# Kernel tuning notes

Hardware: AMD Instinct MI355X
Metric: run time of the kernel (lower is better)

The kernel has to match this reference:

```python
import jax, jax.numpy as jnp
import numpy as np

D_MODEL = 256

def setup_inputs() -> dict:
    key = jax.random.key(0)
    k_x, k_wqkv, k_bqkv, k_wp, k_bp = jax.random.split(key, 5)
    B, T, d = 4, 4096, D_MODEL
    bound_qkv = 1.0 / np.sqrt(d)
    return {
        "x": jax.random.normal(k_x, (B, T, d), dtype=jnp.float32),
        "W_qkv": jax.random.uniform(k_wqkv, (d, 3 * d), jnp.float32, -bound_qkv, bound_qkv),
        "b_qkv": jax.random.uniform(k_bqkv, (3 * d,), jnp.float32, -bound_qkv, bound_qkv),
        "W_proj": jax.random.uniform(k_wp, (d, d), jnp.float32, -bound_qkv, bound_qkv),
        "b_proj": jax.random.uniform(k_bp, (d,), jnp.float32, -bound_qkv, bound_qkv),
    }

def reference(x, W_qkv, b_qkv, W_proj, b_proj):
    B, T, d = x.shape
    qkv = x @ W_qkv + b_qkv                       # (B, T, 3d)
    q, k, v = jnp.split(qkv, 3, axis=-1)          # each (B, T, d)
    scale = 1.0 / np.sqrt(d).astype(np.float32)
    scores = jnp.einsum('btd,bsd->bts', q, k) * scale   # (B, T, T)
    causal = jnp.tril(jnp.ones((T, T), dtype=bool))     # allowed positions
    scores = jnp.where(causal, scores, -jnp.inf)
    weights = jax.nn.softmax(scores, axis=-1)           # (B, T, T)
    ctx = jnp.einsum('bts,bsd->btd', weights, v)        # (B, T, d)
    return ctx @ W_proj + b_proj
```

## Files before the change

kernel.cpp:

```cpp
#include <hip/hip_runtime.h>
#include <math.h>

#define TT 4096
#define BB 4
#define DM 256
#define NSEG_B 288

typedef __attribute__((ext_vector_type(8))) short short8;
typedef __attribute__((ext_vector_type(4))) short short4v;
typedef __attribute__((ext_vector_type(4))) float f32x4;

#define MFMA16(a, b, c) __builtin_amdgcn_mfma_f32_16x16x32_bf16(a, b, c, 0, 0, 0)

#define GL2LDS(gp, lp) __builtin_amdgcn_global_load_lds( \
    (const __attribute__((address_space(1))) unsigned int*)(gp), \
    (__attribute__((address_space(3))) unsigned int*)(lp), 16, 0, 0)

__device__ __forceinline__ short f2b(float f) {
    union { float f; unsigned u; } v; v.f = f;
    unsigned r = v.u + 0x7FFFu + ((v.u >> 16) & 1u);
    return (short)(r >> 16);
}

__global__ __launch_bounds__(256) void transpose_cast2(
    const float* __restrict__ W1, short* __restrict__ Wt1,
    const float* __restrict__ W2, short* __restrict__ Wt2)
{
    __shared__ float T[64 * 68];
    const int tid = threadIdx.x;
    const int by = blockIdx.y;
    const float* W; short* Wt; int N, n0;
    if (by < 12) { W = W1; Wt = Wt1; N = 768; n0 = by * 64; }
    else         { W = W2; Wt = Wt2; N = 256; n0 = (by - 12) * 64; }
    const int k0 = blockIdx.x * 64;
#pragma unroll
    for (int it = 0; it < 4; ++it) {
        int idx = tid + it * 256;
        int r = idx >> 4, c4 = idx & 15;
        *(float4*)&T[r * 68 + c4 * 4] =
            *(const float4*)&W[(size_t)(k0 + r) * N + n0 + c4 * 4];
    }
    __syncthreads();
#pragma unroll
    for (int it = 0; it < 4; ++it) {
        int idx = tid + it * 256;
        int n = idx >> 4, c4 = idx & 15;
        short4v t;
#pragma unroll
        for (int j = 0; j < 4; ++j) t[j] = f2b(T[(c4 * 4 + j) * 68 + n]);
        *(short4v*)&Wt[(size_t)(n0 + n) * 256 + k0 + c4 * 4] = t;
    }
}

__global__ __launch_bounds__(256) void qkv_gemm(
    const float* __restrict__ x, const short* __restrict__ Bt,
    const float* __restrict__ bias, short* __restrict__ qkvb,
    short* __restrict__ VtG)
{
    __shared__ short As[16384];
    __shared__ short Bs[16384];
    __shared__ short Ts[64 * 72];

    const int tid = threadIdx.x;
    const int w = tid >> 6, lane = tid & 63;
    const int l15 = lane & 15, quad = lane >> 4;
    const int m0 = blockIdx.x * 64;
    const int nsup = blockIdx.y * 384;

#pragma unroll
    for (int it = 0; it < 8; ++it) {
        int idx = tid + it * 256;
        int row = ((idx >> 9) << 4) + (idx & 15);
        int col = ((idx >> 6) & 7) * 32 + ((idx >> 4) & 3) * 8;
        const float* src = &x[(size_t)(m0 + row) * 256 + col];
        float4 u = *(const float4*)src, u2 = *(const float4*)(src + 4);
        short8 t;
        t[0] = f2b(u.x);  t[1] = f2b(u.y);  t[2] = f2b(u.z);  t[3] = f2b(u.w);
        t[4] = f2b(u2.x); t[5] = f2b(u2.y); t[6] = f2b(u2.z); t[7] = f2b(u2.w);
        *(short8*)&As[idx * 8] = t;
    }

    for (int t6 = 0; t6 < 6; ++t6) {
        const int n0 = nsup + t6 * 64;
#pragma unroll
        for (int it = 0; it < 8; ++it) {
            int idx = tid + it * 256;
            int n = ((idx >> 9) << 4) + (idx & 15);
            int col = ((idx >> 6) & 7) * 32 + ((idx >> 4) & 3) * 8;
            *(short8*)&Bs[idx * 8] = *(const short8*)&Bt[(size_t)(n0 + n) * 256 + col];
        }
        __syncthreads();

        f32x4 acc[4];
#pragma unroll
        for (int t = 0; t < 4; ++t) acc[t] = (f32x4){0.f, 0.f, 0.f, 0.f};
#pragma unroll
        for (int k0 = 0; k0 < 8; ++k0) {
            short8 a = *(const short8*)&As[((w * 8 + k0) * 64 + lane) * 8];
#pragma unroll
            for (int nt = 0; nt < 4; ++nt) {
                short8 bb = *(const short8*)&Bs[((nt * 8 + k0) * 64 + lane) * 8];
                acc[nt] = MFMA16(a, bb, acc[nt]);
            }
        }

        if (n0 < 512) {
#pragma unroll
            for (int nt = 0; nt < 4; ++nt) {
                int n = n0 + nt * 16 + l15;
                float bv = bias[n];
#pragma unroll
                for (int r = 0; r < 4; ++r)
                    qkvb[(size_t)(m0 + w * 16 + quad * 4 + r) * 768 + n]
                        = f2b(acc[nt][r] + bv);
            }
            __syncthreads();
        } else {
#pragma unroll
            for (int nt = 0; nt < 4; ++nt) {
                int n = n0 + nt * 16 + l15;
                float bv = bias[n];
#pragma unroll
                for (int r = 0; r < 4; ++r)
                    Ts[(nt * 16 + l15) * 72 + w * 16 + quad * 4 + r]
                        = f2b(acc[nt][r] + bv);
            }
            __syncthreads();
            const int d  = tid >> 2;
            const int c  = tid & 3;
            short8 v0 = *(const short8*)&Ts[d * 72 + c * 16];
            short8 v1 = *(const short8*)&Ts[d * 72 + c * 16 + 8];
            const int bg = m0 >> 12, key0 = (m0 & 4095) + c * 16;
            short* dst = &VtG[((size_t)bg * 256 + (n0 - 512) + d) * 4096 + key0];
            *(short8*)dst = v0;
            *(short8*)(dst + 8) = v1;
        }
    }
}

__global__ __launch_bounds__(256, 3) void flash_mfma(
    const short* __restrict__ qkv,
    const short* __restrict__ VtG,
    float* __restrict__ Opart,
    float* __restrict__ L)
{
    __shared__ short Ks[2][4096];
    __shared__ short Vs[2][8192];
    __shared__ short Ps[2048];

    const int tid = threadIdx.x;
    const int w = tid >> 6, lane = tid & 63;
    const int l15 = lane & 15, quad = lane >> 4;

    const int b = blockIdx.x & 3;
    const int e = (NSEG_B - 1) - (blockIdx.x >> 2);
    const int lid = b * NSEG_B + e;
    int g = 0;
    while (g < 7 && e >= 4 * (g + 1) * (g + 2)) ++g;
    int off = e - 4 * g * (g + 1);
    int qt = 8 * g + off / (g + 1);
    int s  = off - (off / (g + 1)) * (g + 1);
    const int kp_lo = s * 16;
    const int kp_hi = min(kp_lo + 16, 2 * (qt + 1));
    const int npairs = kp_hi - kp_lo;

    const size_t base = (size_t)b * TT * 768;
    const int row0 = qt * 64;

    short8 aq[8];
    {
        const short* qrow = &qkv[base + (size_t)(row0 + w * 16 + l15) * 768 + quad * 8];
#pragma unroll
        for (int k0 = 0; k0 < 8; ++k0)
            aq[k0] = *(const short8*)&qrow[k0 * 32];
    }

#pragma unroll
    for (int it = 0; it < 2; ++it) {
        int idx = tid + it * 256;
        int row = idx & 15;
        int col = ((idx >> 6) & 7) * 32 + ((idx >> 4) & 3) * 8;
        GL2LDS(&qkv[base + (size_t)(kp_lo * 32 + row) * 768 + 256 + col], &Ks[0][idx * 8]);
    }
#pragma unroll
    for (int it = 0; it < 4; ++it) {
        int idx = tid + it * 256;
        int d  = ((idx >> 6) << 4) + (idx & 15);
        int kc = ((idx >> 4) & 3) * 8;
        GL2LDS(&VtG[((size_t)b * 256 + d) * 4096 + kp_lo * 32 + kc], &Vs[0][idx * 8]);
    }

    f32x4 o[16];
#pragma unroll
    for (int c = 0; c < 16; ++c) o[c] = (f32x4){0.f, 0.f, 0.f, 0.f};
    float l_acc[4] = {0.f, 0.f, 0.f, 0.f};

    for (int u = 0; u < npairs; ++u) {
        const int j0 = (kp_lo + u) * 32;

        __syncthreads();

#pragma unroll
        for (int it = 0; it < 2; ++it) {
            int idx = tid + it * 256;
            int row = idx & 15;
            int col = ((idx >> 6) & 7) * 32 + ((idx >> 4) & 3) * 8;
            GL2LDS(&qkv[base + (size_t)(j0 + 16 + row) * 768 + 256 + col], &Ks[1][idx * 8]);
        }
        if (u + 1 < npairs) {
#pragma unroll
            for (int it = 0; it < 4; ++it) {
                int idx = tid + it * 256;
                int d  = ((idx >> 6) << 4) + (idx & 15);
                int kc = ((idx >> 4) & 3) * 8;
                GL2LDS(&VtG[((size_t)b * 256 + d) * 4096 + j0 + 32 + kc],
                       &Vs[(u + 1) & 1][idx * 8]);
            }
        }

        {
            f32x4 s4 = (f32x4){0.f, 0.f, 0.f, 0.f};
#pragma unroll
            for (int k0 = 0; k0 < 8; ++k0) {
                short8 bb = *(const short8*)&Ks[0][(k0 * 64 + lane) * 8];
                s4 = MFMA16(aq[k0], bb, s4);
            }
#pragma unroll
            for (int r = 0; r < 4; ++r) {
                const int rg = row0 + w * 16 + quad * 4 + r;
                int jg = j0 + l15;
                float xx = s4[r] * 0.0625f;
                if (jg > rg) xx = -INFINITY;
                float pv = __expf(fminf(xx, 30.f));
                l_acc[r] += pv;
                Ps[(w * 64 + (l15 >> 3) * 16 + quad * 4 + r) * 8 + (l15 & 7)] = f2b(pv);
            }
        }

        __syncthreads();

        if (u + 1 < npairs) {
#pragma unroll
            for (int it = 0; it < 2; ++it) {
                int idx = tid + it * 256;
                int row = idx & 15;
                int col = ((idx >> 6) & 7) * 32 + ((idx >> 4) & 3) * 8;
                GL2LDS(&qkv[base + (size_t)(j0 + 32 + row) * 768 + 256 + col], &Ks[0][idx * 8]);
            }
        }

        {
            f32x4 s4 = (f32x4){0.f, 0.f, 0.f, 0.f};
#pragma unroll
            for (int k0 = 0; k0 < 8; ++k0) {
                short8 bb = *(const short8*)&Ks[1][(k0 * 64 + lane) * 8];
                s4 = MFMA16(aq[k0], bb, s4);
            }
#pragma unroll
            for (int r = 0; r < 4; ++r) {
                const int rg = row0 + w * 16 + quad * 4 + r;
                int jg = j0 + 16 + l15;
                float xx = s4[r] * 0.0625f;
                if (jg > rg) xx = -INFINITY;
                float pv = __expf(fminf(xx, 30.f));
                l_acc[r] += pv;
                Ps[(w * 64 + (2 + (l15 >> 3)) * 16 + quad * 4 + r) * 8 + (l15 & 7)] = f2b(pv);
            }
        }

        {
            short8 a0 = *(const short8*)&Ps[(w * 64 + lane) * 8];
#pragma unroll
            for (int ct = 0; ct < 16; ++ct) {
                short8 bb = *(const short8*)&Vs[u & 1][(ct * 64 + lane) * 8];
                o[ct] = MFMA16(a0, bb, o[ct]);
            }
        }
    }

#pragma unroll
    for (int r = 0; r < 4; ++r) {
        float l = l_acc[r];
        l += __shfl_xor(l, 1); l += __shfl_xor(l, 2);
        l += __shfl_xor(l, 4); l += __shfl_xor(l, 8);
        if (l15 == 0)
            L[(size_t)lid * 64 + w * 16 + quad * 4 + r] = l;
    }
    const size_t ob = (size_t)lid * (64 * 256);
#pragma unroll
    for (int r = 0; r < 4; ++r) {
        int lr = w * 16 + quad * 4 + r;
#pragma unroll
        for (int c = 0; c < 16; ++c)
            Opart[ob + (size_t)lr * 256 + c * 16 + l15] = o[c][r];
    }
}

__global__ __launch_bounds__(256) void proj_gemm(
    const float* __restrict__ Opart, const float* __restrict__ L,
    const short* __restrict__ Bt, const float* __restrict__ bias,
    float* __restrict__ out)
{
    __shared__ short As[16384];
    __shared__ short Bs[16384];
    __shared__ float Linv[64];

    const int tid = threadIdx.x;
    const int w = tid >> 6, lane = tid & 63;
    const int l15 = lane & 15, quad = lane >> 4;
    const int t = blockIdx.x;
    const int b = t >> 6, qt = t & 63;
    const int gg = qt >> 3, rr = qt & 7;
    const int sbase = b * NSEG_B + 4 * gg * (gg + 1) + rr * (gg + 1);
    const int nseg = gg + 1;
    const int m0 = t * 64;

    if (tid < 64) {
        float l = 0.f;
#pragma unroll
        for (int s2 = 0; s2 < 8; ++s2)
            if (s2 < nseg) l += L[(size_t)(sbase + s2) * 64 + tid];
        Linv[tid] = 1.f / l;
    }
    __syncthreads();

#pragma unroll
    for (int it = 0; it < 8; ++it) {
        int idx = tid + it * 256;
        int row = ((idx >> 9) << 4) + (idx & 15);
        int col = ((idx >> 6) & 7) * 32 + ((idx >> 4) & 3) * 8;
        float a8[8] = {0.f, 0.f, 0.f, 0.f, 0.f, 0.f, 0.f, 0.f};
#pragma unroll
        for (int s2 = 0; s2 < 8; ++s2) {
            if (s2 < nseg) {
                const float* src = &Opart[(size_t)(sbase + s2) * 16384
                                          + (size_t)row * 256 + col];
                float4 u = *(const float4*)src, u2 = *(const float4*)(src + 4);
                a8[0] += u.x;  a8[1] += u.y;  a8[2] += u.z;  a8[3] += u.w;
                a8[4] += u2.x; a8[5] += u2.y; a8[6] += u2.z; a8[7] += u2.w;
            }
        }
        float inv = Linv[row];
        short8 t8;
#pragma unroll
        for (int j = 0; j < 8; ++j) t8[j] = f2b(a8[j] * inv);
        *(short8*)&As[idx * 8] = t8;
    }

    for (int t2 = 0; t2 < 2; ++t2) {
        const int n0 = blockIdx.y * 128 + t2 * 64;
#pragma unroll
        for (int it = 0; it < 8; ++it) {
            int idx = tid + it * 256;
            int n = ((idx >> 9) << 4) + (idx & 15);
            int col = ((idx >> 6) & 7) * 32 + ((idx >> 4) & 3) * 8;
            *(short8*)&Bs[idx * 8] = *(const short8*)&Bt[(size_t)(n0 + n) * 256 + col];
        }
        __syncthreads();

        f32x4 acc[4];
#pragma unroll
        for (int tt = 0; tt < 4; ++tt) acc[tt] = (f32x4){0.f, 0.f, 0.f, 0.f};
#pragma unroll
        for (int k0 = 0; k0 < 8; ++k0) {
            short8 a = *(const short8*)&As[((w * 8 + k0) * 64 + lane) * 8];
#pragma unroll
            for (int nt = 0; nt < 4; ++nt) {
                short8 bb = *(const short8*)&Bs[((nt * 8 + k0) * 64 + lane) * 8];
                acc[nt] = MFMA16(a, bb, acc[nt]);
            }
        }
#pragma unroll
        for (int nt = 0; nt < 4; ++nt) {
            int n = n0 + nt * 16 + l15;
            float bv = bias[n];
#pragma unroll
            for (int r = 0; r < 4; ++r)
                out[(size_t)(m0 + w * 16 + quad * 4 + r) * 256 + n] = acc[nt][r] + bv;
        }
        __syncthreads();
    }
}

extern "C" void kernel_launch(void* const* d_in, const int* in_sizes, int n_in,
                              void* d_out, int out_size, void* d_ws, size_t ws_size,
                              hipStream_t stream)
{
    const float* x     = (const float*)d_in[0];
    const float* Wqkv  = (const float*)d_in[1];
    const float* bqkv  = (const float*)d_in[2];
    const float* Wproj = (const float*)d_in[3];
    const float* bproj = (const float*)d_in[4];
    float* out = (float*)d_out;

    const size_t M = (size_t)BB * TT;
    short* qkv_b = (short*)d_ws;
    short* Wt1   = qkv_b + M * 768;
    short* Wt2   = Wt1 + (size_t)768 * 256;
    short* VtG   = Wt2 + (size_t)256 * 256;
    float* Opart = (float*)(VtG + (size_t)BB * 256 * 4096);
    float* L     = Opart + (size_t)BB * NSEG_B * 64 * 256;

    dim3 blk(256);
    transpose_cast2<<<dim3(4, 16), blk, 0, stream>>>(Wqkv, Wt1, Wproj, Wt2);
    qkv_gemm<<<dim3(256, 2), blk, 0, stream>>>(x, Wt1, bqkv, qkv_b, VtG);
    flash_mfma<<<dim3(BB * NSEG_B), blk, 0, stream>>>(qkv_b, VtG, Opart, L);
    proj_gemm<<<dim3(256, 2), blk, 0, stream>>>(Opart, L, Wt2, bproj, out);
}
```

Measured before the change: 226.6 us.

## Widen flash attention tiles to 128 query rows with 512-thread blocks

The flash kernel now processes 128 query rows per block using 8 waves, which halves the number of key/value tile loads per query row and halves the segment count. One block barrier per key pair is replaced by an explicit vmcnt wait plus s_barrier, with sched_barriers to pin the order of async LDS loads relative to compute. The projection GEMM is re-tiled to 32-row blocks covering all 256 output columns to match the new partial layout. The risks are lower occupancy from the larger blocks, fewer blocks to balance across CUs, and fragile hand-written waitcnt counts.

```diff
diff --git a/kernel.cpp b/kernel.cpp
--- a/kernel.cpp
+++ b/kernel.cpp
@@ -4,7 +4,7 @@
 #define TT 4096
 #define BB 4
 #define DM 256
-#define NSEG_B 288
+#define NSEG_B 144
 
 typedef __attribute__((ext_vector_type(8))) short short8;
 typedef __attribute__((ext_vector_type(4))) short short4v;
@@ -138,7 +138,7 @@
     }
 }
 
-__global__ __launch_bounds__(256, 3) void flash_mfma(
+__global__ __launch_bounds__(512, 2) void flash_mfma(
     const short* __restrict__ qkv,
     const short* __restrict__ VtG,
     float* __restrict__ Opart,
@@ -146,7 +146,7 @@
 {
     __shared__ short Ks[2][4096];
     __shared__ short Vs[2][8192];
-    __shared__ short Ps[2048];
+    __shared__ short Ps[4096];
 
     const int tid = threadIdx.x;
     const int w = tid >> 6, lane = tid & 63;
@@ -156,16 +156,16 @@
     const int e = (NSEG_B - 1) - (blockIdx.x >> 2);
     const int lid = b * NSEG_B + e;
     int g = 0;
-    while (g < 7 && e >= 4 * (g + 1) * (g + 2)) ++g;
-    int off = e - 4 * g * (g + 1);
-    int qt = 8 * g + off / (g + 1);
+    while (g < 7 && e >= 2 * (g + 1) * (g + 2)) ++g;
+    int off = e - 2 * g * (g + 1);
+    int qt = 4 * g + off / (g + 1);
     int s  = off - (off / (g + 1)) * (g + 1);
     const int kp_lo = s * 16;
-    const int kp_hi = min(kp_lo + 16, 2 * (qt + 1));
+    const int kp_hi = min(kp_lo + 16, 4 * (qt + 1));
     const int npairs = kp_hi - kp_lo;
 
     const size_t base = (size_t)b * TT * 768;
-    const int row0 = qt * 64;
+    const int row0 = qt * 128;
 
     short8 aq[8];
     {
@@ -175,16 +175,16 @@
             aq[k0] = *(const short8*)&qrow[k0 * 32];
     }
 
-#pragma unroll
-    for (int it = 0; it < 2; ++it) {
-        int idx = tid + it * 256;
+    {
+        int idx = tid;
         int row = idx & 15;
         int col = ((idx >> 6) & 7) * 32 + ((idx >> 4) & 3) * 8;
         GL2LDS(&qkv[base + (size_t)(kp_lo * 32 + row) * 768 + 256 + col], &Ks[0][idx * 8]);
     }
-#pragma unroll
-    for (int it = 0; it < 4; ++it) {
-        int idx = tid + it * 256;
+    __builtin_amdgcn_sched_barrier(0);
+#pragma unroll
+    for (int it = 0; it < 2; ++it) {
+        int idx = tid + it * 512;
         int d  = ((idx >> 6) << 4) + (idx & 15);
         int kc = ((idx >> 4) & 3) * 8;
         GL2LDS(&VtG[((size_t)b * 256 + d) * 4096 + kp_lo * 32 + kc], &Vs[0][idx * 8]);
@@ -200,23 +200,24 @@
 
         __syncthreads();
 
-#pragma unroll
-        for (int it = 0; it < 2; ++it) {
-            int idx = tid + it * 256;
+        {
+            int idx = tid;
             int row = idx & 15;
             int col = ((idx >> 6) & 7) * 32 + ((idx >> 4) & 3) * 8;
             GL2LDS(&qkv[base + (size_t)(j0 + 16 + row) * 768 + 256 + col], &Ks[1][idx * 8]);
         }
+        __builtin_amdgcn_sched_barrier(0);
         if (u + 1 < npairs) {
 #pragma unroll
-            for (int it = 0; it < 4; ++it) {
-                int idx = tid + it * 256;
+            for (int it = 0; it < 2; ++it) {
+                int idx = tid + it * 512;
                 int d  = ((idx >> 6) << 4) + (idx & 15);
                 int kc = ((idx >> 4) & 3) * 8;
                 GL2LDS(&VtG[((size_t)b * 256 + d) * 4096 + j0 + 32 + kc],
                        &Vs[(u + 1) & 1][idx * 8]);
             }
         }
+        __builtin_amdgcn_sched_barrier(0);
 
         {
             f32x4 s4 = (f32x4){0.f, 0.f, 0.f, 0.f};
@@ -237,17 +238,21 @@
             }
         }
 
-        __syncthreads();
-
         if (u + 1 < npairs) {
-#pragma unroll
-            for (int it = 0; it < 2; ++it) {
-                int idx = tid + it * 256;
-                int row = idx & 15;
-                int col = ((idx >> 6) & 7) * 32 + ((idx >> 4) & 3) * 8;
-                GL2LDS(&qkv[base + (size_t)(j0 + 32 + row) * 768 + 256 + col], &Ks[0][idx * 8]);
-            }
-        }
+            asm volatile("s_waitcnt vmcnt(2)" ::: "memory");
+        } else {
+            asm volatile("s_waitcnt vmcnt(0)" ::: "memory");
+        }
+        __builtin_amdgcn_s_barrier();
+        __builtin_amdgcn_sched_barrier(0);
+
+        if (u + 1 < npairs) {
+            int idx = tid;
+            int row = idx & 15;
+            int col = ((idx >> 6) & 7) * 32 + ((idx >> 4) & 3) * 8;
+            GL2LDS(&qkv[base + (size_t)(j0 + 32 + row) * 768 + 256 + col], &Ks[0][idx * 8]);
+        }
+        __builtin_amdgcn_sched_barrier(0);
 
         {
             f32x4 s4 = (f32x4){0.f, 0.f, 0.f, 0.f};
@@ -284,9 +289,9 @@
         l += __shfl_xor(l, 1); l += __shfl_xor(l, 2);
         l += __shfl_xor(l, 4); l += __shfl_xor(l, 8);
         if (l15 == 0)
-            L[(size_t)lid * 64 + w * 16 + quad * 4 + r] = l;
-    }
-    const size_t ob = (size_t)lid * (64 * 256);
+            L[(size_t)lid * 128 + w * 16 + quad * 4 + r] = l;
+    }
+    const size_t ob = (size_t)lid * (128 * 256);
 #pragma unroll
     for (int r = 0; r < 4; ++r) {
         int lr = w * 16 + quad * 4 + r;
@@ -301,31 +306,33 @@
     const short* __restrict__ Bt, const float* __restrict__ bias,
     float* __restrict__ out)
 {
-    __shared__ short As[16384];
+    __shared__ short As[8192];
     __shared__ short Bs[16384];
-    __shared__ float Linv[64];
+    __shared__ float Linv[32];
 
     const int tid = threadIdx.x;
     const int w = tid >> 6, lane = tid & 63;
     const int l15 = lane & 15, quad = lane >> 4;
     const int t = blockIdx.x;
-    const int b = t >> 6, qt = t & 63;
-    const int gg = qt >> 3, rr = qt & 7;
-    const int sbase = b * NSEG_B + 4 * gg * (gg + 1) + rr * (gg + 1);
+    const int b = t >> 7, q32 = t & 127;
+    const int qt = q32 >> 2;
+    const int ro = (q32 & 3) * 32;
+    const int gg = qt >> 2, rr = qt & 3;
+    const int sbase = b * NSEG_B + 2 * gg * (gg + 1) + rr * (gg + 1);
     const int nseg = gg + 1;
-    const int m0 = t * 64;
-
-    if (tid < 64) {
+    const int m0 = t * 32;
+
+    if (tid < 32) {
         float l = 0.f;
 #pragma unroll
         for (int s2 = 0; s2 < 8; ++s2)
-            if (s2 < nseg) l += L[(size_t)(sbase + s2) * 64 + tid];
+            if (s2 < nseg) l += L[(size_t)(sbase + s2) * 128 + ro + tid];
         Linv[tid] = 1.f / l;
     }
     __syncthreads();
 
 #pragma unroll
-    for (int it = 0; it < 8; ++it) {
+    for (int it = 0; it < 4; ++it) {
         int idx = tid + it * 256;
         int row = ((idx >> 9) << 4) + (idx & 15);
         int col = ((idx >> 6) & 7) * 32 + ((idx >> 4) & 3) * 8;
@@ -333,8 +340,8 @@
 #pragma unroll
         for (int s2 = 0; s2 < 8; ++s2) {
             if (s2 < nseg) {
-                const float* src = &Opart[(size_t)(sbase + s2) * 16384
-                                          + (size_t)row * 256 + col];
+                const float* src = &Opart[(size_t)(sbase + s2) * 32768
+                                          + (size_t)(ro + row) * 256 + col];
                 float4 u = *(const float4*)src, u2 = *(const float4*)(src + 4);
                 a8[0] += u.x;  a8[1] += u.y;  a8[2] += u.z;  a8[3] += u.w;
                 a8[4] += u2.x; a8[5] += u2.y; a8[6] += u2.z; a8[7] += u2.w;
@@ -347,8 +354,8 @@
         *(short8*)&As[idx * 8] = t8;
     }
 
-    for (int t2 = 0; t2 < 2; ++t2) {
-        const int n0 = blockIdx.y * 128 + t2 * 64;
+    for (int t2 = 0; t2 < 4; ++t2) {
+        const int n0 = t2 * 64;
 #pragma unroll
         for (int it = 0; it < 8; ++it) {
             int idx = tid + it * 256;
@@ -358,25 +365,26 @@
         }
         __syncthreads();
 
-        f32x4 acc[4];
-#pragma unroll
-        for (int tt = 0; tt < 4; ++tt) acc[tt] = (f32x4){0.f, 0.f, 0.f, 0.f};
+        f32x4 acc[2];
+        acc[0] = (f32x4){0.f, 0.f, 0.f, 0.f};
+        acc[1] = (f32x4){0.f, 0.f, 0.f, 0.f};
 #pragma unroll
         for (int k0 = 0; k0 < 8; ++k0) {
-            short8 a = *(const short8*)&As[((w * 8 + k0) * 64 + lane) * 8];
-#pragma unroll
-            for (int nt = 0; nt < 4; ++nt) {
-                short8 bb = *(const short8*)&Bs[((nt * 8 + k0) * 64 + lane) * 8];
+            short8 a = *(const short8*)&As[(((w & 1) * 8 + k0) * 64 + lane) * 8];
+#pragma unroll
+            for (int nt = 0; nt < 2; ++nt) {
+                int n16 = (w >> 1) * 2 + nt;
+                short8 bb = *(const short8*)&Bs[((n16 * 8 + k0) * 64 + lane) * 8];
                 acc[nt] = MFMA16(a, bb, acc[nt]);
             }
         }
 #pragma unroll
-        for (int nt = 0; nt < 4; ++nt) {
-            int n = n0 + nt * 16 + l15;
+        for (int nt = 0; nt < 2; ++nt) {
+            int n = n0 + ((w >> 1) * 2 + nt) * 16 + l15;
             float bv = bias[n];
 #pragma unroll
             for (int r = 0; r < 4; ++r)
-                out[(size_t)(m0 + w * 16 + quad * 4 + r) * 256 + n] = acc[nt][r] + bv;
+                out[(size_t)(m0 + (w & 1) * 16 + quad * 4 + r) * 256 + n] = acc[nt][r] + bv;
         }
         __syncthreads();
     }
@@ -399,11 +407,10 @@
     short* Wt2   = Wt1 + (size_t)768 * 256;
     short* VtG   = Wt2 + (size_t)256 * 256;
     float* Opart = (float*)(VtG + (size_t)BB * 256 * 4096);
-    float* L     = Opart + (size_t)BB * NSEG_B * 64 * 256;
-
-    dim3 blk(256);
-    transpose_cast2<<<dim3(4, 16), blk, 0, stream>>>(Wqkv, Wt1, Wproj, Wt2);
-    qkv_gemm<<<dim3(256, 2), blk, 0, stream>>>(x, Wt1, bqkv, qkv_b, VtG);
-    flash_mfma<<<dim3(BB * NSEG_B), blk, 0, stream>>>(qkv_b, VtG, Opart, L);
-    proj_gemm<<<dim3(256, 2), blk, 0, stream>>>(Opart, L, Wt2, bproj, out);
-}
+    float* L     = Opart + (size_t)BB * NSEG_B * 128 * 256;
+
+    transpose_cast2<<<dim3(4, 16), dim3(256), 0, stream>>>(Wqkv, Wt1, Wproj, Wt2);
+    qkv_gemm<<<dim3(256, 2), dim3(256), 0, stream>>>(x, Wt1, bqkv, qkv_b, VtG);
+    flash_mfma<<<dim3(BB * NSEG_B), dim3(512), 0, stream>>>(qkv_b, VtG, Opart, L);
+    proj_gemm<<<dim3(512), dim3(256), 0, stream>>>(Opart, L, Wt2, bproj, out);
+}
```

Result: slower. 248.2 us (+9.5%).
